# Optimization experiments

Measured on AMD Instinct MI355X. Metric: run time of the kernel, lower is better.

The kernel has to match this reference:

```python
import jax, jax.numpy as jnp
import numpy as np

B, T, DIN, H, NOUT = 256, 512, 64, 512, 128


def setup_inputs() -> dict:
    key = jax.random.key(0)
    ks = jax.random.split(key, 11)
    s = 1.0 / np.sqrt(H)  # PyTorch GRU init scale
    inp = {"x": jax.random.normal(ks[0], (B, T, DIN), dtype=jnp.float32)}
    # layer 0 (input DIN), layer 1 (input H); gate order: r, z, n
    inp["w_ih0"] = jax.random.uniform(ks[1], (3 * H, DIN), minval=-s, maxval=s)
    inp["w_hh0"] = jax.random.uniform(ks[2], (3 * H, H), minval=-s, maxval=s)
    inp["b_ih0"] = jax.random.uniform(ks[3], (3 * H,), minval=-s, maxval=s)
    inp["b_hh0"] = jax.random.uniform(ks[4], (3 * H,), minval=-s, maxval=s)
    inp["w_ih1"] = jax.random.uniform(ks[5], (3 * H, H), minval=-s, maxval=s)
    inp["w_hh1"] = jax.random.uniform(ks[6], (3 * H, H), minval=-s, maxval=s)
    inp["b_ih1"] = jax.random.uniform(ks[7], (3 * H,), minval=-s, maxval=s)
    inp["b_hh1"] = jax.random.uniform(ks[8], (3 * H,), minval=-s, maxval=s)
    inp["w_fc"] = jax.random.uniform(ks[9], (NOUT, H), minval=-s, maxval=s)
    inp["b_fc"] = jax.random.uniform(ks[10], (NOUT,), minval=-s, maxval=s)
    return inp


def _gru_layer(x_seq, w_ih, w_hh, b_ih, b_hh):
    # x_seq: [B, T, Din] -> hidden trajectory [B, T, H]
    xg = jnp.einsum('btd,gd->btg', x_seq, w_ih) + b_ih  # [B, T, 3H], precomputed input gates
    h0 = jnp.zeros((x_seq.shape[0], w_hh.shape[1]), dtype=x_seq.dtype)

    def step(h, xg_t):
        hg = h @ w_hh.T + b_hh
        xr, xz, xn = jnp.split(xg_t, 3, axis=-1)
        hr, hz, hn = jnp.split(hg, 3, axis=-1)
        r = jax.nn.sigmoid(xr + hr)
        z = jax.nn.sigmoid(xz + hz)
        n = jnp.tanh(xn + r * hn)
        h_new = (1.0 - z) * n + z * h
        return h_new, h_new

    _, hs = jax.lax.scan(step, h0, jnp.swapaxes(xg, 0, 1))  # [T, B, H]
    return jnp.swapaxes(hs, 0, 1)


def reference(x, w_ih0, w_hh0, b_ih0, b_hh0, w_ih1, w_hh1, b_ih1, b_hh1, w_fc, b_fc):
    h1 = _gru_layer(x, w_ih0, w_hh0, b_ih0, b_hh0)   # [B, T, H]
    h2 = _gru_layer(h1, w_ih1, w_hh1, b_ih1, b_hh1)  # [B, T, H]
    last = h2[:, -1, :]                               # [B, H]
    return last @ w_fc.T + b_fc                       # [B, NOUT]
```

## Files before the change

kernel.cpp:

```cpp
#include <hip/hip_runtime.h>
#include <math.h>

typedef unsigned short u16;
typedef __attribute__((ext_vector_type(8))) short s8v;
typedef __attribute__((ext_vector_type(4))) float f4v;
typedef __attribute__((ext_vector_type(4))) int   i4v;

constexpr int kB    = 256;
constexpr int kT    = 512;
constexpr int kDIN  = 64;
constexpr int kH    = 512;
constexpr int kG3   = 1536;
constexpr int kNOUT = 128;
constexpr int kPlane = 8 * 2 * 16 * 512;

__device__ __forceinline__ u16 f2bf(float f) {
  union { float f; unsigned u; } v; v.f = f;
  unsigned r = (v.u + 0x7FFFu + ((v.u >> 16) & 1u)) >> 16;
  return (u16)r;
}
__device__ __forceinline__ float fsig(float x) {
  x = fminf(fmaxf(x, -30.f), 30.f);
  float e = __expf(-x);
  return __fdividef(1.f, 1.f + e);
}
__device__ __forceinline__ float ftanh(float x) {
  x = fminf(fmaxf(x, -15.f), 15.f);
  float e = __expf(-2.f * x);
  return __fdividef(1.f - e, 1.f + e);
}

__device__ __forceinline__ void load_afrag16(const u16* base, i4v a[16]) {
  asm volatile(
      "global_load_dwordx4 %0, %16, off sc0 sc1\n\t"
      "global_load_dwordx4 %1, %16, off offset:1024 sc0 sc1\n\t"
      "global_load_dwordx4 %2, %16, off offset:2048 sc0 sc1\n\t"
      "global_load_dwordx4 %3, %16, off offset:3072 sc0 sc1\n\t"
      "global_load_dwordx4 %4, %17, off sc0 sc1\n\t"
      "global_load_dwordx4 %5, %17, off offset:1024 sc0 sc1\n\t"
      "global_load_dwordx4 %6, %17, off offset:2048 sc0 sc1\n\t"
      "global_load_dwordx4 %7, %17, off offset:3072 sc0 sc1\n\t"
      "global_load_dwordx4 %8, %18, off sc0 sc1\n\t"
      "global_load_dwordx4 %9, %18, off offset:1024 sc0 sc1\n\t"
      "global_load_dwordx4 %10, %18, off offset:2048 sc0 sc1\n\t"
      "global_load_dwordx4 %11, %18, off offset:3072 sc0 sc1\n\t"
      "global_load_dwordx4 %12, %19, off sc0 sc1\n\t"
      "global_load_dwordx4 %13, %19, off offset:1024 sc0 sc1\n\t"
      "global_load_dwordx4 %14, %19, off offset:2048 sc0 sc1\n\t"
      "global_load_dwordx4 %15, %19, off offset:3072 sc0 sc1\n\t"
      "s_waitcnt vmcnt(0)"
      : "=&v"(a[0]), "=&v"(a[1]), "=&v"(a[2]), "=&v"(a[3]),
        "=&v"(a[4]), "=&v"(a[5]), "=&v"(a[6]), "=&v"(a[7]),
        "=&v"(a[8]), "=&v"(a[9]), "=&v"(a[10]), "=&v"(a[11]),
        "=&v"(a[12]), "=&v"(a[13]), "=&v"(a[14]), "=&v"(a[15])
      : "v"(base), "v"(base + 4 * 512), "v"(base + 8 * 512), "v"(base + 12 * 512)
      : "memory");
}

__device__ __forceinline__ void store_h_l0(
    u16* p0, u16* p1, u16* p2, u16* p3,
    u16* q0, u16* q1, u16* q2, u16* q3,
    unsigned v0, unsigned v1, unsigned v2, unsigned v3) {
  asm volatile(
      "global_store_short %0, %8, off sc0 sc1\n\t"
      "global_store_short %1, %9, off sc0 sc1\n\t"
      "global_store_short %2, %10, off sc0 sc1\n\t"
      "global_store_short %3, %11, off sc0 sc1\n\t"
      "global_store_short %4, %8, off\n\t"
      "global_store_short %5, %9, off\n\t"
      "global_store_short %6, %10, off\n\t"
      "global_store_short %7, %11, off\n\t"
      "s_waitcnt vmcnt(4)"
      :: "v"(p0), "v"(p1), "v"(p2), "v"(p3),
         "v"(q0), "v"(q1), "v"(q2), "v"(q3),
         "v"(v0), "v"(v1), "v"(v2), "v"(v3)
      : "memory");
}
__device__ __forceinline__ void store_h_l1(
    u16* p0, u16* p1, u16* p2, u16* p3,
    unsigned v0, unsigned v1, unsigned v2, unsigned v3) {
  asm volatile(
      "global_store_short %0, %4, off sc0 sc1\n\t"
      "global_store_short %1, %5, off sc0 sc1\n\t"
      "global_store_short %2, %6, off sc0 sc1\n\t"
      "global_store_short %3, %7, off sc0 sc1\n\t"
      "s_waitcnt vmcnt(0)"
      :: "v"(p0), "v"(p1), "v"(p2), "v"(p3),
         "v"(v0), "v"(v1), "v"(v2), "v"(v3)
      : "memory");
}

__global__ void build_wslab(const float* __restrict__ w, u16* __restrict__ d) {
  int idx  = blockIdx.x * 256 + threadIdx.x;
  int lane = idx & 63, fg = idx >> 6;
  int jt = fg / 96, f = fg % 96;
  int nt = f >> 4, kt = f & 15;
  int g = nt >> 1, u = nt & 1;
  int row = g * 512 + jt * 32 + u * 16 + (lane & 15);
  int k0  = kt * 32 + (lane >> 4) * 8;
  const float* src = w + (size_t)row * 512 + k0;
  u16* dst = d + ((size_t)fg) * 512 + lane * 8;
#pragma unroll
  for (int i = 0; i < 8; i++) dst[i] = f2bf(src[i]);
}

__global__ __launch_bounds__(256, 1)
void coop_rec(int c, int TC, int nc, unsigned bar_base16, unsigned* bar,
              const float* __restrict__ xg0, const float* __restrict__ xg1,
              const u16* __restrict__ wslab0, const u16* __restrict__ wslab1,
              const float* __restrict__ bhh0, const float* __restrict__ bhh1,
              u16* __restrict__ h1seq, u16* __restrict__ hbuf,
              float* __restrict__ carry) {
  const int bid   = blockIdx.x;
  const int layer = bid >> 7;
  const int lb    = bid & 127;
  const int jt    = lb & 15, bt = lb >> 4;
  const int cc    = (layer == 0) ? c : c - 1;
  const bool active = (cc >= 0 && cc < nc);

  unsigned* mybar = bar + (size_t)(layer * 8 + bt) * 64;

  if (!active) {
    if (threadIdx.x == 0)
      __hip_atomic_fetch_add(mybar, (unsigned)TC, __ATOMIC_RELAXED,
                             __HIP_MEMORY_SCOPE_AGENT);
    return;
  }

  const float* xg    = layer ? xg1 : xg0;
  const u16*  wslab  = layer ? wslab1 : wslab0;
  const float* bhh   = layer ? bhh1 : bhh0;
  float* mycarry = carry + (size_t)layer * kB * kH;

  const int tid  = threadIdx.x;
  const int wv   = tid >> 6, lane = tid & 63;
  const int mt   = wv >> 1, u = wv & 1;
  const int b0   = bt * 32;
  const int jl   = lane & 15;
  const int jg   = jt * 32 + u * 16 + jl;
  const int mrow = (lane >> 4) * 4;

  s8v bfr[3][16];
  {
    const u16* base = wslab + (size_t)jt * 96 * 512;
#pragma unroll
    for (int g = 0; g < 3; ++g)
#pragma unroll
      for (int kt = 0; kt < 16; ++kt)
        bfr[g][kt] = *(const s8v*)&base[(size_t)((g * 2 + u) * 16 + kt) * 512 + lane * 8];
  }
  const float bh_r = bhh[jg], bh_z = bhh[512 + jg], bh_n = bhh[1024 + jg];

  float hp[4];
#pragma unroll
  for (int r = 0; r < 4; ++r)
    hp[r] = mycarry[(size_t)(b0 + mt * 16 + mrow + r) * 512 + jg];

  const size_t cons_off = ((size_t)((bt * 2 + mt) * 16)) * 512 + lane * 8;
  const size_t prod_off = ((size_t)((bt * 2 + mt) * 16 + jt)) * 512 +
                          (size_t)(16 * (u * 2 + (jl >> 3))) * 8 + (jl & 7);
  const int bbase = b0 + mt * 16 + mrow;

  float xv0[4], xv1[4], xv2[4];
  auto prefetch_xg = [&](int tt) {
#pragma unroll
    for (int r = 0; r < 4; ++r) {
      const float* xp = xg + ((size_t)(bbase + r) * TC + tt) * kG3;
      xv0[r] = xp[jg]; xv1[r] = xp[512 + jg]; xv2[r] = xp[1024 + jg];
    }
  };
  prefetch_xg(0);

  for (int t = 0; t < TC; ++t) {
    if (tid == 0) {
      unsigned tgt = bar_base16 + 16u * (unsigned)t;
      int guard = 0;
      while (__hip_atomic_load(mybar, __ATOMIC_RELAXED,
                               __HIP_MEMORY_SCOPE_AGENT) < tgt
             && ++guard < (1 << 21)) {
        __builtin_amdgcn_s_sleep(1);
      }
    }
    __syncthreads();

    const u16* plane = hbuf + (size_t)(layer * 2 + (t & 1)) * kPlane;
    i4v a[16];
    load_afrag16(plane + cons_off, a);

    f4v acc0 = {0.f, 0.f, 0.f, 0.f}, acc1 = acc0, acc2 = acc0;
#pragma unroll
    for (int kt = 0; kt < 16; ++kt) {
      const s8v av = __builtin_bit_cast(s8v, a[kt]);
      acc0 = __builtin_amdgcn_mfma_f32_16x16x32_bf16(av, bfr[0][kt], acc0, 0, 0, 0);
      acc1 = __builtin_amdgcn_mfma_f32_16x16x32_bf16(av, bfr[1][kt], acc1, 0, 0, 0);
      acc2 = __builtin_amdgcn_mfma_f32_16x16x32_bf16(av, bfr[2][kt], acc2, 0, 0, 0);
    }

    unsigned hv[4];
#pragma unroll
    for (int r = 0; r < 4; ++r) {
      float rr = fsig(xv0[r] + acc0[r] + bh_r);
      float zz = fsig(xv1[r] + acc1[r] + bh_z);
      float nn = ftanh(xv2[r] + rr * (acc2[r] + bh_n));
      float hn = (1.f - zz) * nn + zz * hp[r];
      hp[r] = hn;
      hv[r] = f2bf(hn);
    }

    u16* pb = hbuf + (size_t)(layer * 2 + ((t + 1) & 1)) * kPlane + prod_off;
    if (layer == 0) {
      u16* q = h1seq + ((size_t)bbase * TC + t) * 512 + jg;
      store_h_l0(pb + (size_t)(mrow + 0) * 8, pb + (size_t)(mrow + 1) * 8,
                 pb + (size_t)(mrow + 2) * 8, pb + (size_t)(mrow + 3) * 8,
                 q, q + (size_t)TC * 512, q + 2 * (size_t)TC * 512,
                 q + 3 * (size_t)TC * 512,
                 hv[0], hv[1], hv[2], hv[3]);
    } else {
      store_h_l1(pb + (size_t)(mrow + 0) * 8, pb + (size_t)(mrow + 1) * 8,
                 pb + (size_t)(mrow + 2) * 8, pb + (size_t)(mrow + 3) * 8,
                 hv[0], hv[1], hv[2], hv[3]);
    }
    __syncthreads();
    if (tid == 0)
      __hip_atomic_fetch_add(mybar, 1u, __ATOMIC_RELAXED,
                             __HIP_MEMORY_SCOPE_AGENT);
    if (t + 1 < TC) prefetch_xg(t + 1);
  }

#pragma unroll
  for (int r = 0; r < 4; ++r)
    mycarry[(size_t)(bbase + r) * 512 + jg] = hp[r];
}

__device__ void gemm_role(int idx, int TC,
                          const float* __restrict__ Af, const u16* __restrict__ Ab,
                          int Abstride, int Atoff, int K,
                          const float* __restrict__ Bf, const float* __restrict__ bias,
                          float* __restrict__ C, char* smem) {
  u16* As = (u16*)smem;
  u16* Bs = As + 128 * 40;
  const int tid = threadIdx.x;
  const int mt = idx / 12, nt = idx % 12;
  const int m0 = mt * 128, n0 = nt * 128;
  const int w = tid >> 6, lane = tid & 63;
  const int wm = w & 1, wn = w >> 1;
  const int ra = tid >> 2, koff = (tid & 3) * 8;

  const int r = m0 + ra;
  const size_t aoff = ((size_t)(r / TC) * Abstride + Atoff + (r % TC)) * K;
  const float* arowF = Af ? Af + aoff : nullptr;
  const u16*  arowB = Ab ? Ab + aoff : nullptr;
  const float* browF = Bf + (size_t)(n0 + ra) * K;

  f4v acc[4][2];
#pragma unroll
  for (int i = 0; i < 4; i++)
#pragma unroll
    for (int jn = 0; jn < 2; jn++) acc[i][jn] = (f4v){0.f, 0.f, 0.f, 0.f};

  for (int k0 = 0; k0 < K; k0 += 32) {
    s8v av, bv;
    if (arowB) {
      av = *(const s8v*)(arowB + k0 + koff);
    } else {
      u16 tmp[8];
      const float* ap = arowF + k0 + koff;
#pragma unroll
      for (int i = 0; i < 8; i++) tmp[i] = f2bf(ap[i]);
      av = *(s8v*)tmp;
    }
    {
      u16 tmp[8];
      const float* bp = browF + k0 + koff;
#pragma unroll
      for (int i = 0; i < 8; i++) tmp[i] = f2bf(bp[i]);
      bv = *(s8v*)tmp;
    }
    __syncthreads();
    *(s8v*)&As[ra * 40 + koff] = av;
    *(s8v*)&Bs[ra * 40 + koff] = bv;
    __syncthreads();
    s8v af[4];
#pragma unroll
    for (int i = 0; i < 4; i++)
      af[i] = *(const s8v*)&As[(wm * 64 + i * 16 + (lane & 15)) * 40 + (lane >> 4) * 8];
#pragma unroll
    for (int jn = 0; jn < 2; jn++) {
      s8v bf = *(const s8v*)&Bs[(wn * 32 + jn * 16 + (lane & 15)) * 40 + (lane >> 4) * 8];
#pragma unroll
      for (int i = 0; i < 4; i++)
        acc[i][jn] = __builtin_amdgcn_mfma_f32_16x16x32_bf16(af[i], bf, acc[i][jn], 0, 0, 0);
    }
  }

#pragma unroll
  for (int jn = 0; jn < 2; jn++) {
    int n = n0 + wn * 32 + jn * 16 + (lane & 15);
    float bv2 = bias[n];
#pragma unroll
    for (int i = 0; i < 4; i++) {
      int mrow = m0 + wm * 64 + i * 16 + (lane >> 4) * 4;
#pragma unroll
      for (int reg = 0; reg < 4; reg++)
        C[(size_t)(mrow + reg) * kG3 + n] = acc[i][jn][reg] + bv2;
    }
  }
}

__global__ __launch_bounds__(512)
void gemm_kernel(int TC, const float* Af, const u16* Ab, int Abstride, int Atoff,
                 int K, const float* Bf, const float* bias, float* C) {
  __shared__ __align__(16) char smem[2 * 128 * 40 * 2];
  gemm_role(blockIdx.x, TC, Af, Ab, Abstride, Atoff, K, Bf, bias, C, smem);
}

__global__ __launch_bounds__(512)
void gemm2_kernel(int TC, int G1, int do0,
                  const float* x, int atoff0, const u16* h1seq,
                  const float* wih0, const float* bih0, float* xg0,
                  const float* wih1, const float* bih1, float* xg1) {
  __shared__ __align__(16) char smem[2 * 128 * 40 * 2];
  if ((int)blockIdx.x < G1) {
    gemm_role(blockIdx.x, TC, nullptr, h1seq, TC, 0, kH, wih1, bih1, xg1, smem);
  } else if (do0) {
    gemm_role(blockIdx.x - G1, TC, x, nullptr, kT, atoff0, kDIN, wih0, bih0,
              xg0, smem);
  }
}

__global__ __launch_bounds__(128)
void fc_kernel(const float* __restrict__ h, const float* __restrict__ wfc,
               const float* __restrict__ bfc, float* __restrict__ out) {
  const int b = blockIdx.x;
  const int n = threadIdx.x;
  const float* hrow = h + (size_t)b * kH;
  const float* wrow = wfc + (size_t)n * kH;
  float acc = 0.f;
#pragma unroll 4
  for (int k = 0; k < kH; k += 4) {
    const float4 hv = *(const float4*)&hrow[k];
    const float4 wv = *(const float4*)&wrow[k];
    acc = fmaf(hv.x, wv.x, acc); acc = fmaf(hv.y, wv.y, acc);
    acc = fmaf(hv.z, wv.z, acc); acc = fmaf(hv.w, wv.w, acc);
  }
  out[(size_t)b * kNOUT + n] = acc + bfc[n];
}

extern "C" void kernel_launch(void* const* d_in, const int* in_sizes, int n_in,
                              void* d_out, int out_size, void* d_ws, size_t ws_size,
                              hipStream_t stream) {
  const float* x     = (const float*)d_in[0];
  const float* w_ih0 = (const float*)d_in[1];
  const float* w_hh0 = (const float*)d_in[2];
  const float* b_ih0 = (const float*)d_in[3];
  const float* b_hh0 = (const float*)d_in[4];
  const float* w_ih1 = (const float*)d_in[5];
  const float* w_hh1 = (const float*)d_in[6];
  const float* b_ih1 = (const float*)d_in[7];
  const float* b_hh1 = (const float*)d_in[8];
  const float* w_fc  = (const float*)d_in[9];
  const float* b_fc  = (const float*)d_in[10];
  float* out = (float*)d_out;

  auto need = [](int tc) -> size_t {
    size_t s = 0;
    s += 2 * (size_t)kB * tc * kG3 * 4;
    s += (size_t)kB * tc * kH * 2;
    s += 2 * (size_t)kG3 * kH * 2;
    s += 4 * (size_t)kPlane * 2;
    s += 2 * (size_t)kB * kH * 4;
    s += 32768;
    return s;
  };
  int TC = 64;
  while (TC > 2 && need(TC) > ws_size) TC >>= 1;
  const int nc = kT / TC;

  char* p = (char*)d_ws;
  auto carve = [&](size_t bytes) {
    char* r = p; p += (bytes + 255) & ~(size_t)255; return r;
  };
  float* xg0   = (float*)carve((size_t)kB * TC * kG3 * 4);
  float* xg1   = (float*)carve((size_t)kB * TC * kG3 * 4);
  u16* h1seq   = (u16*)carve((size_t)kB * TC * kH * 2);
  u16* wslab0  = (u16*)carve((size_t)kG3 * kH * 2);
  u16* wslab1  = (u16*)carve((size_t)kG3 * kH * 2);
  u16* hbuf    = (u16*)carve(4 * (size_t)kPlane * 2);
  float* carry = (float*)carve(2 * (size_t)kB * kH * 4);
  unsigned* bar = (unsigned*)carve(32 * 64 * sizeof(unsigned));

  build_wslab<<<384, 256, 0, stream>>>(w_hh0, wslab0);
  build_wslab<<<384, 256, 0, stream>>>(w_hh1, wslab1);
  hipMemsetAsync(hbuf, 0, 4 * (size_t)kPlane * 2 + 2 * (size_t)kB * kH * 4, stream);
  hipMemsetAsync(bar, 0, 32 * 64 * sizeof(unsigned), stream);

  const int G1 = 24 * TC;

  gemm_kernel<<<dim3(G1), 512, 0, stream>>>(TC, x, nullptr, kT, 0, kDIN,
                                            w_ih0, b_ih0, xg0);

  for (int c = 0; c <= nc; ++c) {
    unsigned base16 = (unsigned)c * 16u * (unsigned)TC;
    coop_rec<<<dim3(256), dim3(256), 0, stream>>>(
        c, TC, nc, base16, bar, xg0, xg1, wslab0, wslab1,
        b_hh0, b_hh1, h1seq, hbuf, carry);
    if (c < nc) {
      int do0 = (c + 1 < nc) ? 1 : 0;
      gemm2_kernel<<<dim3(2 * G1), 512, 0, stream>>>(
          TC, G1, do0, x, (c + 1) * TC, h1seq,
          w_ih0, b_ih0, xg0, w_ih1, b_ih1, xg1);
    }
  }

  fc_kernel<<<dim3(kB), dim3(kNOUT), 0, stream>>>(
      carry + (size_t)kB * kH, w_fc, b_fc, out);
}
```

Baseline: 2.612 ms.

## Fuse recurrence and input-projection GEMMs into one wavefront-pipelined kernel

```diff
diff --git a/kernel.cpp b/kernel.cpp
--- a/kernel.cpp
+++ b/kernel.cpp
@@ -18,6 +18,9 @@
   union { float f; unsigned u; } v; v.f = f;
   unsigned r = (v.u + 0x7FFFu + ((v.u >> 16) & 1u)) >> 16;
   return (u16)r;
+}
+__device__ __forceinline__ float bf2f(u16 u) {
+  union { unsigned u; float f; } v; v.u = ((unsigned)u) << 16; return v.f;
 }
 __device__ __forceinline__ float fsig(float x) {
   x = fminf(fmaxf(x, -30.f), 30.f);
@@ -104,32 +107,13 @@
   for (int i = 0; i < 8; i++) dst[i] = f2bf(src[i]);
 }
 
-__global__ __launch_bounds__(256, 1)
-void coop_rec(int c, int TC, int nc, unsigned bar_base16, unsigned* bar,
-              const float* __restrict__ xg0, const float* __restrict__ xg1,
-              const u16* __restrict__ wslab0, const u16* __restrict__ wslab1,
-              const float* __restrict__ bhh0, const float* __restrict__ bhh1,
-              u16* __restrict__ h1seq, u16* __restrict__ hbuf,
-              float* __restrict__ carry) {
-  const int bid   = blockIdx.x;
-  const int layer = bid >> 7;
-  const int lb    = bid & 127;
-  const int jt    = lb & 15, bt = lb >> 4;
-  const int cc    = (layer == 0) ? c : c - 1;
-  const bool active = (cc >= 0 && cc < nc);
-
-  unsigned* mybar = bar + (size_t)(layer * 8 + bt) * 64;
-
-  if (!active) {
-    if (threadIdx.x == 0)
-      __hip_atomic_fetch_add(mybar, (unsigned)TC, __ATOMIC_RELAXED,
-                             __HIP_MEMORY_SCOPE_AGENT);
-    return;
-  }
-
-  const float* xg    = layer ? xg1 : xg0;
-  const u16*  wslab  = layer ? wslab1 : wslab0;
-  const float* bhh   = layer ? bhh1 : bhh0;
+__device__ void rec_role(int layer, int TC, unsigned bar_base16,
+                         unsigned* mybar, int bt, int jt,
+                         const u16* __restrict__ xg,
+                         const u16* __restrict__ wslab,
+                         const float* __restrict__ bhh,
+                         u16* __restrict__ h1p,
+                         u16* __restrict__ hbuf, float* __restrict__ carry) {
   float* mycarry = carry + (size_t)layer * kB * kH;
 
   const int tid  = threadIdx.x;
@@ -161,12 +145,12 @@
                           (size_t)(16 * (u * 2 + (jl >> 3))) * 8 + (jl & 7);
   const int bbase = b0 + mt * 16 + mrow;
 
-  float xv0[4], xv1[4], xv2[4];
+  u16 xu0[4], xu1[4], xu2[4];
   auto prefetch_xg = [&](int tt) {
 #pragma unroll
     for (int r = 0; r < 4; ++r) {
-      const float* xp = xg + ((size_t)(bbase + r) * TC + tt) * kG3;
-      xv0[r] = xp[jg]; xv1[r] = xp[512 + jg]; xv2[r] = xp[1024 + jg];
+      const u16* xp = xg + ((size_t)(bbase + r) * TC + tt) * kG3;
+      xu0[r] = xp[jg]; xu1[r] = xp[512 + jg]; xu2[r] = xp[1024 + jg];
     }
   };
   prefetch_xg(0);
@@ -199,9 +183,9 @@
     unsigned hv[4];
 #pragma unroll
     for (int r = 0; r < 4; ++r) {
-      float rr = fsig(xv0[r] + acc0[r] + bh_r);
-      float zz = fsig(xv1[r] + acc1[r] + bh_z);
-      float nn = ftanh(xv2[r] + rr * (acc2[r] + bh_n));
+      float rr = fsig(bf2f(xu0[r]) + acc0[r] + bh_r);
+      float zz = fsig(bf2f(xu1[r]) + acc1[r] + bh_z);
+      float nn = ftanh(bf2f(xu2[r]) + rr * (acc2[r] + bh_n));
       float hn = (1.f - zz) * nn + zz * hp[r];
       hp[r] = hn;
       hv[r] = f2bf(hn);
@@ -209,7 +193,7 @@
 
     u16* pb = hbuf + (size_t)(layer * 2 + ((t + 1) & 1)) * kPlane + prod_off;
     if (layer == 0) {
-      u16* q = h1seq + ((size_t)bbase * TC + t) * 512 + jg;
+      u16* q = h1p + ((size_t)bbase * TC + t) * 512 + jg;
       store_h_l0(pb + (size_t)(mrow + 0) * 8, pb + (size_t)(mrow + 1) * 8,
                  pb + (size_t)(mrow + 2) * 8, pb + (size_t)(mrow + 3) * 8,
                  q, q + (size_t)TC * 512, q + 2 * (size_t)TC * 512,
@@ -232,25 +216,25 @@
     mycarry[(size_t)(bbase + r) * 512 + jg] = hp[r];
 }
 
-__device__ void gemm_role(int idx, int TC,
-                          const float* __restrict__ Af, const u16* __restrict__ Ab,
-                          int Abstride, int Atoff, int K,
-                          const float* __restrict__ Bf, const float* __restrict__ bias,
-                          float* __restrict__ C, char* smem) {
+__device__ void gemm64x128(int idx, int TC,
+                           const float* __restrict__ Af, const u16* __restrict__ Ab,
+                           int Abstride, int Atoff, int K,
+                           const float* __restrict__ W, const float* __restrict__ bias,
+                           u16* __restrict__ Cb, char* smem) {
   u16* As = (u16*)smem;
-  u16* Bs = As + 128 * 40;
+  u16* Bs = As + 64 * 40;
   const int tid = threadIdx.x;
   const int mt = idx / 12, nt = idx % 12;
-  const int m0 = mt * 128, n0 = nt * 128;
+  const int m0 = mt * 64, n0 = nt * 128;
   const int w = tid >> 6, lane = tid & 63;
-  const int wm = w & 1, wn = w >> 1;
   const int ra = tid >> 2, koff = (tid & 3) * 8;
 
   const int r = m0 + ra;
   const size_t aoff = ((size_t)(r / TC) * Abstride + Atoff + (r % TC)) * K;
   const float* arowF = Af ? Af + aoff : nullptr;
   const u16*  arowB = Ab ? Ab + aoff : nullptr;
-  const float* browF = Bf + (size_t)(n0 + ra) * K;
+  const float* brow0 = W + (size_t)(n0 + ra) * K;
+  const float* brow1 = W + (size_t)(n0 + ra + 64) * K;
 
   f4v acc[4][2];
 #pragma unroll
@@ -259,7 +243,7 @@
     for (int jn = 0; jn < 2; jn++) acc[i][jn] = (f4v){0.f, 0.f, 0.f, 0.f};
 
   for (int k0 = 0; k0 < K; k0 += 32) {
-    s8v av, bv;
+    s8v av, bv0, bv1;
     if (arowB) {
       av = *(const s8v*)(arowB + k0 + koff);
     } else {
@@ -270,23 +254,25 @@
       av = *(s8v*)tmp;
     }
     {
-      u16 tmp[8];
-      const float* bp = browF + k0 + koff;
-#pragma unroll
-      for (int i = 0; i < 8; i++) tmp[i] = f2bf(bp[i]);
-      bv = *(s8v*)tmp;
+      u16 t0[8], t1[8];
+      const float* bp0 = brow0 + k0 + koff;
+      const float* bp1 = brow1 + k0 + koff;
+#pragma unroll
+      for (int i = 0; i < 8; i++) { t0[i] = f2bf(bp0[i]); t1[i] = f2bf(bp1[i]); }
+      bv0 = *(s8v*)t0; bv1 = *(s8v*)t1;
     }
     __syncthreads();
     *(s8v*)&As[ra * 40 + koff] = av;
-    *(s8v*)&Bs[ra * 40 + koff] = bv;
+    *(s8v*)&Bs[ra * 40 + koff] = bv0;
+    *(s8v*)&Bs[(ra + 64) * 40 + koff] = bv1;
     __syncthreads();
     s8v af[4];
 #pragma unroll
     for (int i = 0; i < 4; i++)
-      af[i] = *(const s8v*)&As[(wm * 64 + i * 16 + (lane & 15)) * 40 + (lane >> 4) * 8];
+      af[i] = *(const s8v*)&As[(i * 16 + (lane & 15)) * 40 + (lane >> 4) * 8];
 #pragma unroll
     for (int jn = 0; jn < 2; jn++) {
-      s8v bf = *(const s8v*)&Bs[(wn * 32 + jn * 16 + (lane & 15)) * 40 + (lane >> 4) * 8];
+      s8v bf = *(const s8v*)&Bs[(w * 32 + jn * 16 + (lane & 15)) * 40 + (lane >> 4) * 8];
 #pragma unroll
       for (int i = 0; i < 4; i++)
         acc[i][jn] = __builtin_amdgcn_mfma_f32_16x16x32_bf16(af[i], bf, acc[i][jn], 0, 0, 0);
@@ -295,37 +281,71 @@
 
 #pragma unroll
   for (int jn = 0; jn < 2; jn++) {
-    int n = n0 + wn * 32 + jn * 16 + (lane & 15);
+    int n = n0 + w * 32 + jn * 16 + (lane & 15);
     float bv2 = bias[n];
 #pragma unroll
     for (int i = 0; i < 4; i++) {
-      int mrow = m0 + wm * 64 + i * 16 + (lane >> 4) * 4;
+      int mr = m0 + i * 16 + (lane >> 4) * 4;
 #pragma unroll
       for (int reg = 0; reg < 4; reg++)
-        C[(size_t)(mrow + reg) * kG3 + n] = acc[i][jn][reg] + bv2;
-    }
-  }
-}
-
-__global__ __launch_bounds__(512)
-void gemm_kernel(int TC, const float* Af, const u16* Ab, int Abstride, int Atoff,
-                 int K, const float* Bf, const float* bias, float* C) {
-  __shared__ __align__(16) char smem[2 * 128 * 40 * 2];
-  gemm_role(blockIdx.x, TC, Af, Ab, Abstride, Atoff, K, Bf, bias, C, smem);
-}
-
-__global__ __launch_bounds__(512)
-void gemm2_kernel(int TC, int G1, int do0,
-                  const float* x, int atoff0, const u16* h1seq,
-                  const float* wih0, const float* bih0, float* xg0,
-                  const float* wih1, const float* bih1, float* xg1) {
-  __shared__ __align__(16) char smem[2 * 128 * 40 * 2];
-  if ((int)blockIdx.x < G1) {
-    gemm_role(blockIdx.x, TC, nullptr, h1seq, TC, 0, kH, wih1, bih1, xg1, smem);
-  } else if (do0) {
-    gemm_role(blockIdx.x - G1, TC, x, nullptr, kT, atoff0, kDIN, wih0, bih0,
-              xg0, smem);
-  }
+        Cb[(size_t)(mr + reg) * kG3 + n] = f2bf(acc[i][jn][reg] + bv2);
+    }
+  }
+}
+
+__global__ __launch_bounds__(256, 1)
+void mega(int c, int TC, int nc, unsigned bar_base16, unsigned* bar,
+          const float* __restrict__ x,
+          u16* __restrict__ xg0, u16* __restrict__ xg1,
+          u16* __restrict__ h1seq,
+          const u16* __restrict__ wslab0, const u16* __restrict__ wslab1,
+          const float* __restrict__ bhh0, const float* __restrict__ bhh1,
+          const float* __restrict__ wih0, const float* __restrict__ bih0,
+          const float* __restrict__ wih1, const float* __restrict__ bih1,
+          u16* __restrict__ hbuf, float* __restrict__ carry) {
+  __shared__ __align__(16) char smem[(64 + 128) * 40 * 2];
+  const int bid = blockIdx.x;
+  const int G1  = 48 * TC;
+  const size_t xgChunk = (size_t)kB * TC * kG3;
+  const size_t h1Chunk = (size_t)kB * TC * kH;
+  const int par = c & 1;
+
+  if (bid < 256) {
+    const int layer = bid >> 7;
+    const int lb    = bid & 127;
+    const int jt    = lb & 15, bt = lb >> 4;
+    const int cc    = layer ? c - 2 : c;
+    unsigned* mybar = bar + (size_t)(layer * 8 + bt) * 64;
+    if (cc < 0 || cc >= nc) {
+      if (threadIdx.x == 0)
+        __hip_atomic_fetch_add(mybar, (unsigned)TC, __ATOMIC_RELAXED,
+                               __HIP_MEMORY_SCOPE_AGENT);
+      return;
+    }
+    const u16* xg = (layer ? xg1 : xg0) + (size_t)par * xgChunk;
+    u16* h1p = (layer == 0) ? (h1seq + (size_t)par * h1Chunk) : nullptr;
+    rec_role(layer, TC, bar_base16, mybar, bt, jt, xg,
+             layer ? wslab1 : wslab0, layer ? bhh1 : bhh0,
+             h1p, hbuf, carry);
+  } else if (bid < 256 + G1) {
+    const int cc = c - 1;
+    if (cc < 0 || cc >= nc) return;
+    gemm64x128(bid - 256, TC, nullptr, h1seq + (size_t)(cc & 1) * h1Chunk,
+               TC, 0, kH, wih1, bih1, xg1 + (size_t)(cc & 1) * xgChunk, smem);
+  } else {
+    const int cc = c + 1;
+    if (cc < 1 || cc >= nc) return;
+    gemm64x128(bid - 256 - G1, TC, x, nullptr, kT, cc * TC, kDIN,
+               wih0, bih0, xg0 + (size_t)(cc & 1) * xgChunk, smem);
+  }
+}
+
+__global__ __launch_bounds__(256)
+void proj0_kernel(int TC, const float* __restrict__ x,
+                  const float* __restrict__ wih0, const float* __restrict__ bih0,
+                  u16* __restrict__ xg0) {
+  __shared__ __align__(16) char smem[(64 + 128) * 40 * 2];
+  gemm64x128(blockIdx.x, TC, x, nullptr, kT, 0, kDIN, wih0, bih0, xg0, smem);
 }
 
 __global__ __launch_bounds__(128)
@@ -364,8 +384,9 @@
 
   auto need = [](int tc) -> size_t {
     size_t s = 0;
-    s += 2 * (size_t)kB * tc * kG3 * 4;
-    s += (size_t)kB * tc * kH * 2;
+    s += 2 * (size_t)kB * tc * kG3 * 2;
+    s += 2 * (size_t)kB * tc * kG3 * 2;
+    s += 2 * (size_t)kB * tc * kH * 2;
     s += 2 * (size_t)kG3 * kH * 2;
     s += 4 * (size_t)kPlane * 2;
     s += 2 * (size_t)kB * kH * 4;
@@ -380,9 +401,9 @@
   auto carve = [&](size_t bytes) {
     char* r = p; p += (bytes + 255) & ~(size_t)255; return r;
   };
-  float* xg0   = (float*)carve((size_t)kB * TC * kG3 * 4);
-  float* xg1   = (float*)carve((size_t)kB * TC * kG3 * 4);
-  u16* h1seq   = (u16*)carve((size_t)kB * TC * kH * 2);
+  u16* xg0     = (u16*)carve(2 * (size_t)kB * TC * kG3 * 2);
+  u16* xg1     = (u16*)carve(2 * (size_t)kB * TC * kG3 * 2);
+  u16* h1seq   = (u16*)carve(2 * (size_t)kB * TC * kH * 2);
   u16* wslab0  = (u16*)carve((size_t)kG3 * kH * 2);
   u16* wslab1  = (u16*)carve((size_t)kG3 * kH * 2);
   u16* hbuf    = (u16*)carve(4 * (size_t)kPlane * 2);
@@ -394,22 +415,15 @@
   hipMemsetAsync(hbuf, 0, 4 * (size_t)kPlane * 2 + 2 * (size_t)kB * kH * 4, stream);
   hipMemsetAsync(bar, 0, 32 * 64 * sizeof(unsigned), stream);
 
-  const int G1 = 24 * TC;
-
-  gemm_kernel<<<dim3(G1), 512, 0, stream>>>(TC, x, nullptr, kT, 0, kDIN,
-                                            w_ih0, b_ih0, xg0);
-
-  for (int c = 0; c <= nc; ++c) {
+  proj0_kernel<<<dim3(48 * TC), 256, 0, stream>>>(TC, x, w_ih0, b_ih0, xg0);
+
+  const dim3 grid(256 + 2 * 48 * TC);
+  for (int c = 0; c <= nc + 1; ++c) {
     unsigned base16 = (unsigned)c * 16u * (unsigned)TC;
-    coop_rec<<<dim3(256), dim3(256), 0, stream>>>(
-        c, TC, nc, base16, bar, xg0, xg1, wslab0, wslab1,
-        b_hh0, b_hh1, h1seq, hbuf, carry);
-    if (c < nc) {
-      int do0 = (c + 1 < nc) ? 1 : 0;
-      gemm2_kernel<<<dim3(2 * G1), 512, 0, stream>>>(
-          TC, G1, do0, x, (c + 1) * TC, h1seq,
-          w_ih0, b_ih0, xg0, w_ih1, b_ih1, xg1);
-    }
+    mega<<<grid, 256, 0, stream>>>(
+        c, TC, nc, base16, bar, x, xg0, xg1, h1seq,
+        wslab0, wslab1, b_hh0, b_hh1,
+        w_ih0, b_ih0, w_ih1, b_ih1, hbuf, carry);
   }
 
   fc_kernel<<<dim3(kB), dim3(kNOUT), 0, stream>>>(
```

New measurement: 3.515 ms. 1.35x slower.
